# Optimization experiments

Hardware: AMD Instinct MI355X
Metric: run time of the kernel (lower is better)

Reference implementation:

```python
import math
import jax, jax.numpy as jnp
import numpy as np

D_MODEL = 1024
HEADS = 16
B, S = 4, 2048


def setup_inputs() -> dict:
    key = jax.random.key(0)
    ks = jax.random.split(key, 8)
    scale = 1.0 / math.sqrt(D_MODEL)
    return {
        "q": jax.random.normal(ks[0], (B, S, D_MODEL), dtype=jnp.float32),
        "k": jax.random.normal(ks[1], (B, S, D_MODEL), dtype=jnp.float32),
        "v": jax.random.normal(ks[2], (B, S, D_MODEL), dtype=jnp.float32),
        "mask": jax.random.randint(ks[3], (B, S), 0, 2).astype(jnp.bool_),
        "alibi_mask": jax.random.normal(ks[4], (1, HEADS, S, S), dtype=jnp.float32),
        "Wq": jax.random.normal(ks[5], (D_MODEL, D_MODEL), dtype=jnp.float32) * scale,
        "Wk": jax.random.normal(ks[6], (D_MODEL, D_MODEL), dtype=jnp.float32) * scale,
        "Wv": jax.random.normal(ks[7], (D_MODEL, D_MODEL), dtype=jnp.float32) * scale,
    }


def _split_heads(x):
    b, s, d = x.shape
    return x.reshape(b, s, HEADS, d // HEADS).transpose(0, 2, 1, 3)  # [B,H,S,hd]


def reference(q, k, v, mask, alibi_mask, Wq, Wk, Wv):
    # QKV projections (Linear, no bias)
    qh = _split_heads(q @ Wq)
    kh = _split_heads(k @ Wk)
    vh = _split_heads(v @ Wv)
    depth = qh.shape[-1]
    # naive full attention matrix [B,H,Sq,Sk]
    w = jnp.einsum("bhqd,bhkd->bhqk", qh, kh) / math.sqrt(depth)
    # mask: [B,Sk] -> [B,1,1,Sk], True = masked
    w = jnp.where(mask[:, None, None, :], -jnp.inf, w)
    w = w + alibi_mask
    a = jax.nn.softmax(w, axis=-1)  # dropout p=0 -> identity
    out = jnp.einsum("bhqk,bhkd->bhqd", a, vh)
    # combine heads -> [B,S,D]
    out = out.transpose(0, 2, 1, 3).reshape(q.shape[0], q.shape[1], -1)
    return (out, a)
```

## Files before the change

### kernel.cpp

```cpp
#include <hip/hip_runtime.h>
#include <hip/hip_bf16.h>
#include <math.h>

constexpr int B  = 4;
constexpr int S  = 2048;
constexpr int D  = 1024;
constexpr int H  = 16;
constexpr int HD = 64;
constexpr float SCALE = 0.125f;

using f32x4 = __attribute__((ext_vector_type(4))) float;
using s16x8 = __attribute__((ext_vector_type(8))) short;
using u16x8 = __attribute__((ext_vector_type(8))) unsigned short;
using u16x4 = __attribute__((ext_vector_type(4))) unsigned short;

__device__ __forceinline__ unsigned short f2bf(float f) {
    union { float f; unsigned u; } x; x.f = f;
    unsigned r = x.u + 0x7fffu + ((x.u >> 16) & 1u);
    return (unsigned short)(r >> 16);
}
__device__ __forceinline__ float bf2f(unsigned short h) {
    union { unsigned u; float f; } x; x.u = ((unsigned)h) << 16;
    return x.f;
}

#define MFMA_BF16(Af, Bf, Cf) __builtin_amdgcn_mfma_f32_16x16x32_bf16(Af, Bf, Cf, 0, 0, 0)

__global__ __launch_bounds__(256) void k_wt(const float* __restrict__ W,
                                            unsigned short* __restrict__ Wt) {
    __shared__ unsigned short T[64][68];
    const int k0 = blockIdx.x * 64, n0 = blockIdx.y * 64;
    const int t = threadIdx.x;
    {
        const int kr = t >> 4, nc4 = (t & 15) * 4;
        for (int rr = 0; rr < 4; ++rr) {
            const int kk = kr + rr * 16;
            f32x4 wv = *reinterpret_cast<const f32x4*>(&W[(size_t)(k0 + kk) * D + n0 + nc4]);
#pragma unroll
            for (int j = 0; j < 4; ++j) T[nc4 + j][kk] = f2bf(wv[j]);
        }
    }
    __syncthreads();
    {
        const int nr = t >> 4, kc4 = (t & 15) * 4;
        for (int rr = 0; rr < 4; ++rr) {
            const int nn = nr + rr * 16;
            u16x4 o;
#pragma unroll
            for (int j = 0; j < 4; ++j) o[j] = T[nn][kc4 + j];
            *reinterpret_cast<u16x4*>(&Wt[(size_t)(n0 + nn) * D + k0 + kc4]) = o;
        }
    }
}

__global__ __launch_bounds__(256) void k_proj_mfma(const float* __restrict__ X,
                                                   const unsigned short* __restrict__ Wt,
                                                   unsigned short* __restrict__ Y) {
    __shared__ alignas(16) unsigned short As[128][72];
    __shared__ alignas(16) unsigned short Bs[128][72];
    const int bm = blockIdx.y * 128, bn = blockIdx.x * 128;
    const int t = threadIdx.x, w = t >> 6, l = t & 63;
    const int wr = w >> 1, wc = w & 1;
    const int lr = l & 15, lg = l >> 4;
    f32x4 acc[4][4] = {};

    for (int k0 = 0; k0 < D; k0 += 64) {
        {
            const int c4 = (t & 15) * 4;
            int row = t >> 4;
            for (int rr = 0; rr < 8; ++rr, row += 16) {
                f32x4 xv = *reinterpret_cast<const f32x4*>(&X[(size_t)(bm + row) * D + k0 + c4]);
                u16x4 hv;
#pragma unroll
                for (int j = 0; j < 4; ++j) hv[j] = f2bf(xv[j]);
                *reinterpret_cast<u16x4*>(&As[row][c4]) = hv;
            }
        }
        for (int i = 0; i < 4; ++i) {
            const int idx = t + i * 256;
            const int row = idx >> 3, c8 = (idx & 7) * 8;
            *reinterpret_cast<u16x8*>(&Bs[row][c8]) =
                *reinterpret_cast<const u16x8*>(&Wt[(size_t)(bn + row) * D + k0 + c8]);
        }
        __syncthreads();
#pragma unroll
        for (int kk = 0; kk < 2; ++kk) {
            s16x8 af[4], bf[4];
#pragma unroll
            for (int f = 0; f < 4; ++f) {
                af[f] = *reinterpret_cast<const s16x8*>(&As[wr * 64 + f * 16 + lr][kk * 32 + lg * 8]);
                bf[f] = *reinterpret_cast<const s16x8*>(&Bs[wc * 64 + f * 16 + lr][kk * 32 + lg * 8]);
            }
#pragma unroll
            for (int fm = 0; fm < 4; ++fm)
#pragma unroll
                for (int fn = 0; fn < 4; ++fn)
                    acc[fm][fn] = MFMA_BF16(af[fm], bf[fn], acc[fm][fn]);
        }
        __syncthreads();
    }
#pragma unroll
    for (int fm = 0; fm < 4; ++fm)
#pragma unroll
        for (int fn = 0; fn < 4; ++fn)
#pragma unroll
            for (int r = 0; r < 4; ++r) {
                const int m = bm + wr * 64 + fm * 16 + lg * 4 + r;
                const int n = bn + wc * 64 + fn * 16 + lr;
                const int b = m >> 11, s = m & (S - 1);
                const int h = n >> 6, e = n & 63;
                Y[(((size_t)(b * H + h) * S) + s) * HD + e] = f2bf(acc[fm][fn][r]);
            }
}

__global__ __launch_bounds__(256) void k_vt(const unsigned short* __restrict__ Vh,
                                            unsigned short* __restrict__ VT) {
    __shared__ alignas(16) unsigned short T[64][264];
    const int bh = blockIdx.y;
    const int s0 = blockIdx.x * 256;
    const int t = threadIdx.x;
    {
        const int e4 = (t & 15) * 4;
        int sr = t >> 4;
        for (int rr = 0; rr < 16; ++rr, sr += 16) {
            u16x4 vv = *reinterpret_cast<const u16x4*>(&Vh[((size_t)bh * S + s0 + sr) * HD + e4]);
#pragma unroll
            for (int j = 0; j < 4; ++j) T[e4 + j][sr] = vv[j];
        }
    }
    __syncthreads();
    {
        const int e = t >> 2, sl0 = (t & 3) * 64;
        for (int c = 0; c < 8; ++c) {
            u16x8 o = *reinterpret_cast<const u16x8*>(&T[e][sl0 + c * 8]);
            *reinterpret_cast<u16x8*>(&VT[((size_t)bh * HD + e) * S + s0 + sl0 + c * 8]) = o;
        }
    }
}

__global__ __launch_bounds__(256) void k_abf16(const float* __restrict__ A,
                                               unsigned short* __restrict__ O) {
    const size_t N = (size_t)H * S * S;
    const size_t stride = (size_t)gridDim.x * 256 * 8;
    for (size_t i = ((size_t)blockIdx.x * 256 + threadIdx.x) * 8; i < N; i += stride) {
        f32x4 a0 = *reinterpret_cast<const f32x4*>(&A[i]);
        f32x4 a1 = *reinterpret_cast<const f32x4*>(&A[i + 4]);
        u16x8 o;
#pragma unroll
        for (int j = 0; j < 4; ++j) { o[j] = f2bf(a0[j]); o[4 + j] = f2bf(a1[j]); }
        *reinterpret_cast<u16x8*>(&O[i]) = o;
    }
}

template <bool ABF16>
__global__ __launch_bounds__(512, 4) void k_sumexp(
    const unsigned short* __restrict__ QH, const unsigned short* __restrict__ KH,
    const float* __restrict__ ALIBI, const unsigned short* __restrict__ ABF,
    const int* __restrict__ MASK, float* __restrict__ INVL) {
    __shared__ alignas(16) unsigned short Ks[64][72];
    __shared__ alignas(16) unsigned short ALs[128][72];

    const int bh = blockIdx.y, b = bh >> 4, h = bh & 15;
    const int q0 = blockIdx.x * 128;
    const int t = threadIdx.x, w = t >> 6, ln = t & 63;
    const int lr = ln & 15, lg = ln >> 4;

    const unsigned short* Qb = QH + (size_t)bh * S * HD;
    const unsigned short* Kb = KH + (size_t)bh * S * HD;
    const size_t hoff = (size_t)h * S * S;

    s16x8 qf[2];
#pragma unroll
    for (int kk = 0; kk < 2; ++kk)
        qf[kk] = *reinterpret_cast<const s16x8*>(
            &Qb[(size_t)(q0 + w * 16 + lr) * HD + kk * 32 + lg * 8]);

    float psum[4] = {0.f, 0.f, 0.f, 0.f};

    for (int k0 = 0; k0 < S; k0 += 64) {
        {
            const int row = t >> 3, c8 = (t & 7) * 8;
            *reinterpret_cast<u16x8*>(&Ks[row][c8]) =
                *reinterpret_cast<const u16x8*>(&Kb[(size_t)(k0 + row) * HD + c8]);
        }
#pragma unroll
        for (int i = 0; i < 2; ++i) {
            const int idx = t + i * 512, row = idx >> 3, c8 = (idx & 7) * 8;
            u16x8 av;
            if constexpr (ABF16) {
                av = *reinterpret_cast<const u16x8*>(&ABF[hoff + (size_t)(q0 + row) * S + k0 + c8]);
            } else {
                f32x4 a0 = *reinterpret_cast<const f32x4*>(&ALIBI[hoff + (size_t)(q0 + row) * S + k0 + c8]);
                f32x4 a1 = *reinterpret_cast<const f32x4*>(&ALIBI[hoff + (size_t)(q0 + row) * S + k0 + c8 + 4]);
#pragma unroll
                for (int j = 0; j < 4; ++j) { av[j] = f2bf(a0[j]); av[4 + j] = f2bf(a1[j]); }
            }
            *reinterpret_cast<u16x8*>(&ALs[row][c8]) = av;
        }
        float madd[4];
#pragma unroll
        for (int fn = 0; fn < 4; ++fn)
            madd[fn] = MASK[b * S + k0 + fn * 16 + lr] ? -1e30f : 0.f;
        __syncthreads();

        f32x4 acc[4] = {};
#pragma unroll
        for (int kk = 0; kk < 2; ++kk)
#pragma unroll
            for (int fn = 0; fn < 4; ++fn) {
                s16x8 kf = *reinterpret_cast<const s16x8*>(&Ks[fn * 16 + lr][kk * 32 + lg * 8]);
                acc[fn] = MFMA_BF16(qf[kk], kf, acc[fn]);
            }
#pragma unroll
        for (int r = 0; r < 4; ++r) {
            const int rowl = w * 16 + lg * 4 + r;
            float s = 0.f;
#pragma unroll
            for (int fn = 0; fn < 4; ++fn)
                s += __expf(fmaf(acc[fn][r], SCALE, bf2f(ALs[rowl][fn * 16 + lr]) + madd[fn]));
            psum[r] += s;
        }
        __syncthreads();
    }

#pragma unroll
    for (int r = 0; r < 4; ++r) {
        float ps = psum[r];
#pragma unroll
        for (int off = 1; off < 16; off <<= 1) ps += __shfl_xor(ps, off, 64);
        if (lr == 0)
            INVL[(size_t)bh * S + q0 + w * 16 + lg * 4 + r] = 1.0f / ps;
    }
}

template <bool ABF16>
__global__ __launch_bounds__(512, 2) void k_attn(
    const unsigned short* __restrict__ QH, const unsigned short* __restrict__ KH,
    const unsigned short* __restrict__ VT, const float* __restrict__ ALIBI,
    const unsigned short* __restrict__ ABF, const int* __restrict__ MASK,
    const float* __restrict__ INVL, float* __restrict__ Aout,
    float* __restrict__ OUT) {
    __shared__ alignas(16) unsigned short Ps[128][72];
    __shared__ alignas(16) unsigned short Ks[64][72];
    __shared__ alignas(16) unsigned short Vs[64][72];
    __shared__ alignas(16) unsigned short ALs[128][72];

    const int bh = blockIdx.y, b = bh >> 4, h = bh & 15;
    const int q0 = blockIdx.x * 128;
    const int t = threadIdx.x, w = t >> 6, ln = t & 63;
    const int lr = ln & 15, lg = ln >> 4;

    const unsigned short* Qb = QH + (size_t)bh * S * HD;
    const unsigned short* Kb = KH + (size_t)bh * S * HD;
    const unsigned short* Vb = VT + (size_t)bh * HD * S;
    const size_t hoff = (size_t)h * S * S;

    s16x8 qf[2];
#pragma unroll
    for (int kk = 0; kk < 2; ++kk)
        qf[kk] = *reinterpret_cast<const s16x8*>(
            &Qb[(size_t)(q0 + w * 16 + lr) * HD + kk * 32 + lg * 8]);

    float invl[4];
#pragma unroll
    for (int r = 0; r < 4; ++r)
        invl[r] = INVL[(size_t)bh * S + q0 + w * 16 + lg * 4 + r];

    f32x4 oacc[4] = {};
    for (int k0 = 0; k0 < S; k0 += 64) {
        {
            const int row = t >> 3, c8 = (t & 7) * 8;
            *reinterpret_cast<u16x8*>(&Ks[row][c8]) =
                *reinterpret_cast<const u16x8*>(&Kb[(size_t)(k0 + row) * HD + c8]);
            *reinterpret_cast<u16x8*>(&Vs[row][c8]) =
                *reinterpret_cast<const u16x8*>(&Vb[(size_t)row * S + k0 + c8]);
        }
#pragma unroll
        for (int i = 0; i < 2; ++i) {
            const int idx = t + i * 512, row = idx >> 3, c8 = (idx & 7) * 8;
            u16x8 av;
            if constexpr (ABF16) {
                av = *reinterpret_cast<const u16x8*>(&ABF[hoff + (size_t)(q0 + row) * S + k0 + c8]);
            } else {
                f32x4 a0 = *reinterpret_cast<const f32x4*>(&ALIBI[hoff + (size_t)(q0 + row) * S + k0 + c8]);
                f32x4 a1 = *reinterpret_cast<const f32x4*>(&ALIBI[hoff + (size_t)(q0 + row) * S + k0 + c8 + 4]);
#pragma unroll
                for (int j = 0; j < 4; ++j) { av[j] = f2bf(a0[j]); av[4 + j] = f2bf(a1[j]); }
            }
            *reinterpret_cast<u16x8*>(&ALs[row][c8]) = av;
        }
        float madd[4];
#pragma unroll
        for (int fn = 0; fn < 4; ++fn)
            madd[fn] = MASK[b * S + k0 + fn * 16 + lr] ? -1e30f : 0.f;
        __syncthreads();

        f32x4 acc[4] = {};
#pragma unroll
        for (int kk = 0; kk < 2; ++kk)
#pragma unroll
            for (int fn = 0; fn < 4; ++fn) {
                s16x8 kf = *reinterpret_cast<const s16x8*>(&Ks[fn * 16 + lr][kk * 32 + lg * 8]);
                acc[fn] = MFMA_BF16(qf[kk], kf, acc[fn]);
            }
#pragma unroll
        for (int r = 0; r < 4; ++r) {
            const int rowl = w * 16 + lg * 4 + r;
#pragma unroll
            for (int fn = 0; fn < 4; ++fn) {
                float p = __expf(fmaf(acc[fn][r], SCALE,
                                      bf2f(ALs[rowl][fn * 16 + lr]) + madd[fn])) * invl[r];
                Ps[rowl][fn * 16 + lr] = f2bf(p);
            }
        }
        __syncthreads();

#pragma unroll
        for (int i = 0; i < 2; ++i) {
            const int idx = t + i * 512, row = idx >> 3, sub = idx & 7;
            u16x8 pv = *reinterpret_cast<const u16x8*>(&Ps[row][sub * 8]);
            f32x4 o0, o1;
#pragma unroll
            for (int j = 0; j < 4; ++j) { o0[j] = bf2f(pv[j]); o1[j] = bf2f(pv[4 + j]); }
            float* dst = &Aout[((size_t)bh * S + q0 + row) * S + k0 + sub * 8];
            *reinterpret_cast<f32x4*>(dst) = o0;
            *reinterpret_cast<f32x4*>(dst + 4) = o1;
        }
#pragma unroll
        for (int c = 0; c < 2; ++c) {
            s16x8 pa = *reinterpret_cast<const s16x8*>(&Ps[w * 16 + lr][c * 32 + lg * 8]);
#pragma unroll
            for (int fn = 0; fn < 4; ++fn) {
                s16x8 vf = *reinterpret_cast<const s16x8*>(&Vs[fn * 16 + lr][c * 32 + lg * 8]);
                oacc[fn] = MFMA_BF16(pa, vf, oacc[fn]);
            }
        }
        __syncthreads();
    }

#pragma unroll
    for (int fn = 0; fn < 4; ++fn)
#pragma unroll
        for (int r = 0; r < 4; ++r)
            OUT[(size_t)(b * S + q0 + w * 16 + lg * 4 + r) * D + h * HD + fn * 16 + lr] =
                oacc[fn][r];
}

extern "C" void kernel_launch(void* const* d_in, const int* in_sizes, int n_in,
                              void* d_out, int out_size, void* d_ws, size_t ws_size,
                              hipStream_t stream) {
    const float* q     = (const float*)d_in[0];
    const float* k     = (const float*)d_in[1];
    const float* v     = (const float*)d_in[2];
    const int*   mask  = (const int*)d_in[3];
    const float* alibi = (const float*)d_in[4];
    const float* Wq    = (const float*)d_in[5];
    const float* Wk    = (const float*)d_in[6];
    const float* Wv    = (const float*)d_in[7];

    float* out = (float*)d_out;
    float* a   = out + (size_t)B * S * D;

    const size_t NH = (size_t)B * H * S * HD;
    unsigned short* qh  = (unsigned short*)d_ws;
    unsigned short* kh  = qh + NH;
    unsigned short* vh  = kh + NH;
    unsigned short* vT  = vh + NH;
    unsigned short* wqt = vT + NH;
    unsigned short* wkt = wqt + (size_t)D * D;
    unsigned short* wvt = wkt + (size_t)D * D;
    float*          invl = (float*)(wvt + (size_t)D * D);
    unsigned short* abf  = (unsigned short*)(invl + (size_t)B * H * S);

    const size_t need_bf16 =
        ((size_t)((unsigned short*)abf - qh) + (size_t)H * S * S) * sizeof(unsigned short);
    const bool use_abf16 = ws_size >= need_bf16;

    const dim3 blk(256);

    k_wt<<<dim3(D / 64, D / 64), blk, 0, stream>>>(Wq, wqt);
    k_wt<<<dim3(D / 64, D / 64), blk, 0, stream>>>(Wk, wkt);
    k_wt<<<dim3(D / 64, D / 64), blk, 0, stream>>>(Wv, wvt);

    if (use_abf16)
        k_abf16<<<dim3(8192), blk, 0, stream>>>(alibi, abf);

    k_proj_mfma<<<dim3(D / 128, (B * S) / 128), blk, 0, stream>>>(q, wqt, qh);
    k_proj_mfma<<<dim3(D / 128, (B * S) / 128), blk, 0, stream>>>(k, wkt, kh);
    k_proj_mfma<<<dim3(D / 128, (B * S) / 128), blk, 0, stream>>>(v, wvt, vh);

    k_vt<<<dim3(S / 256, B * H), blk, 0, stream>>>(vh, vT);

    if (use_abf16) {
        k_sumexp<true><<<dim3(S / 128, B * H), dim3(512), 0, stream>>>(
            qh, kh, alibi, abf, mask, invl);
        k_attn<true><<<dim3(S / 128, B * H), dim3(512), 0, stream>>>(
            qh, kh, vT, alibi, abf, mask, invl, a, out);
    } else {
        k_sumexp<false><<<dim3(S / 128, B * H), dim3(512), 0, stream>>>(
            qh, kh, alibi, abf, mask, invl);
        k_attn<false><<<dim3(S / 128, B * H), dim3(512), 0, stream>>>(
            qh, kh, vT, alibi, abf, mask, invl, a, out);
    }
}
```

Before: 714.3 us.

## Fuse V transpose into projection, batch-share alibi in sumexp, double-buffer attention

The V projection now writes its transposed layout directly through shared memory, which removes the separate transpose kernel and the intermediate V buffer. The sumexp kernel walks all four batches for each head and query tile, so each alibi tile is read and converted once and shared across batches. That kernel also writes the bf16 alibi copy itself, replacing the standalone conversion kernel. The attention kernel double-buffers K/V tiles, remaps block indices into an XCD-aware order, raises the occupancy hint, and writes the probability matrix with nontemporal fp32 stores straight from registers. In exchange, sumexp launches only 256 blocks, which may leave compute units underused, and it holds more registers for four query fragment sets.

```diff
diff --git a/kernel.cpp b/kernel.cpp
--- a/kernel.cpp
+++ b/kernel.cpp
@@ -113,225 +113,279 @@
             }
 }
 
-__global__ __launch_bounds__(256) void k_vt(const unsigned short* __restrict__ Vh,
-                                            unsigned short* __restrict__ VT) {
-    __shared__ alignas(16) unsigned short T[64][264];
-    const int bh = blockIdx.y;
-    const int s0 = blockIdx.x * 256;
-    const int t = threadIdx.x;
-    {
-        const int e4 = (t & 15) * 4;
-        int sr = t >> 4;
-        for (int rr = 0; rr < 16; ++rr, sr += 16) {
-            u16x4 vv = *reinterpret_cast<const u16x4*>(&Vh[((size_t)bh * S + s0 + sr) * HD + e4]);
-#pragma unroll
-            for (int j = 0; j < 4; ++j) T[e4 + j][sr] = vv[j];
-        }
-    }
+__global__ __launch_bounds__(256) void k_projv_mfma(const float* __restrict__ X,
+                                                    const unsigned short* __restrict__ Wt,
+                                                    unsigned short* __restrict__ VT) {
+    __shared__ alignas(16) unsigned short SM[2][128][72];
+    unsigned short (*As)[72] = SM[0];
+    unsigned short (*Bs)[72] = SM[1];
+    const int bm = blockIdx.y * 128, bn = blockIdx.x * 128;
+    const int t = threadIdx.x, w = t >> 6, l = t & 63;
+    const int wr = w >> 1, wc = w & 1;
+    const int lr = l & 15, lg = l >> 4;
+    f32x4 acc[4][4] = {};
+
+    for (int k0 = 0; k0 < D; k0 += 64) {
+        {
+            const int c4 = (t & 15) * 4;
+            int row = t >> 4;
+            for (int rr = 0; rr < 8; ++rr, row += 16) {
+                f32x4 xv = *reinterpret_cast<const f32x4*>(&X[(size_t)(bm + row) * D + k0 + c4]);
+                u16x4 hv;
+#pragma unroll
+                for (int j = 0; j < 4; ++j) hv[j] = f2bf(xv[j]);
+                *reinterpret_cast<u16x4*>(&As[row][c4]) = hv;
+            }
+        }
+        for (int i = 0; i < 4; ++i) {
+            const int idx = t + i * 256;
+            const int row = idx >> 3, c8 = (idx & 7) * 8;
+            *reinterpret_cast<u16x8*>(&Bs[row][c8]) =
+                *reinterpret_cast<const u16x8*>(&Wt[(size_t)(bn + row) * D + k0 + c8]);
+        }
+        __syncthreads();
+#pragma unroll
+        for (int kk = 0; kk < 2; ++kk) {
+            s16x8 af[4], bf[4];
+#pragma unroll
+            for (int f = 0; f < 4; ++f) {
+                af[f] = *reinterpret_cast<const s16x8*>(&As[wr * 64 + f * 16 + lr][kk * 32 + lg * 8]);
+                bf[f] = *reinterpret_cast<const s16x8*>(&Bs[wc * 64 + f * 16 + lr][kk * 32 + lg * 8]);
+            }
+#pragma unroll
+            for (int fm = 0; fm < 4; ++fm)
+#pragma unroll
+                for (int fn = 0; fn < 4; ++fn)
+                    acc[fm][fn] = MFMA_BF16(af[fm], bf[fn], acc[fm][fn]);
+        }
+        __syncthreads();
+    }
+    unsigned short (*T)[144] = reinterpret_cast<unsigned short(*)[144]>(&SM[0][0][0]);
+#pragma unroll
+    for (int fm = 0; fm < 4; ++fm)
+#pragma unroll
+        for (int fn = 0; fn < 4; ++fn)
+#pragma unroll
+            for (int r = 0; r < 4; ++r)
+                T[wc * 64 + fn * 16 + lr][wr * 64 + fm * 16 + lg * 4 + r] = f2bf(acc[fm][fn][r]);
     __syncthreads();
-    {
-        const int e = t >> 2, sl0 = (t & 3) * 64;
-        for (int c = 0; c < 8; ++c) {
-            u16x8 o = *reinterpret_cast<const u16x8*>(&T[e][sl0 + c * 8]);
-            *reinterpret_cast<u16x8*>(&VT[((size_t)bh * HD + e) * S + s0 + sl0 + c * 8]) = o;
-        }
-    }
-}
-
-__global__ __launch_bounds__(256) void k_abf16(const float* __restrict__ A,
-                                               unsigned short* __restrict__ O) {
-    const size_t N = (size_t)H * S * S;
-    const size_t stride = (size_t)gridDim.x * 256 * 8;
-    for (size_t i = ((size_t)blockIdx.x * 256 + threadIdx.x) * 8; i < N; i += stride) {
-        f32x4 a0 = *reinterpret_cast<const f32x4*>(&A[i]);
-        f32x4 a1 = *reinterpret_cast<const f32x4*>(&A[i + 4]);
-        u16x8 o;
-#pragma unroll
-        for (int j = 0; j < 4; ++j) { o[j] = f2bf(a0[j]); o[4 + j] = f2bf(a1[j]); }
-        *reinterpret_cast<u16x8*>(&O[i]) = o;
+    const int b = bm >> 11, s0 = bm & (S - 1);
+    for (int it = 0; it < 8; ++it) {
+        const int idx = t + it * 256;
+        const int row = idx >> 4, c8 = (idx & 15) * 8;
+        const int h = (bn + row) >> 6, e = (bn + row) & 63;
+        *reinterpret_cast<u16x8*>(&VT[((size_t)(b * H + h) * HD + e) * S + s0 + c8]) =
+            *reinterpret_cast<const u16x8*>(&T[row][c8]);
     }
 }
 
 template <bool ABF16>
 __global__ __launch_bounds__(512, 4) void k_sumexp(
     const unsigned short* __restrict__ QH, const unsigned short* __restrict__ KH,
-    const float* __restrict__ ALIBI, const unsigned short* __restrict__ ABF,
+    const float* __restrict__ ALIBI, unsigned short* __restrict__ ABF,
     const int* __restrict__ MASK, float* __restrict__ INVL) {
-    __shared__ alignas(16) unsigned short Ks[64][72];
-    __shared__ alignas(16) unsigned short ALs[128][72];
-
-    const int bh = blockIdx.y, b = bh >> 4, h = bh & 15;
-    const int q0 = blockIdx.x * 128;
+    __shared__ alignas(16) unsigned short Ks[2][64][72];
+    __shared__ alignas(16) unsigned short ALs[2][128][72];
+
+    const int bid = blockIdx.x;
+    const int wg = (bid & 7) * 32 + (bid >> 3);
+    const int h = wg >> 4;
+    const int q0 = (wg & 15) * 128;
     const int t = threadIdx.x, w = t >> 6, ln = t & 63;
     const int lr = ln & 15, lg = ln >> 4;
-
-    const unsigned short* Qb = QH + (size_t)bh * S * HD;
-    const unsigned short* Kb = KH + (size_t)bh * S * HD;
     const size_t hoff = (size_t)h * S * S;
 
-    s16x8 qf[2];
-#pragma unroll
-    for (int kk = 0; kk < 2; ++kk)
-        qf[kk] = *reinterpret_cast<const s16x8*>(
-            &Qb[(size_t)(q0 + w * 16 + lr) * HD + kk * 32 + lg * 8]);
-
-    float psum[4] = {0.f, 0.f, 0.f, 0.f};
-
-    for (int k0 = 0; k0 < S; k0 += 64) {
-        {
-            const int row = t >> 3, c8 = (t & 7) * 8;
-            *reinterpret_cast<u16x8*>(&Ks[row][c8]) =
-                *reinterpret_cast<const u16x8*>(&Kb[(size_t)(k0 + row) * HD + c8]);
-        }
+    s16x8 qf[4][2];
+#pragma unroll
+    for (int b = 0; b < 4; ++b)
+#pragma unroll
+        for (int kk = 0; kk < 2; ++kk)
+            qf[b][kk] = *reinterpret_cast<const s16x8*>(
+                &QH[((size_t)(b * H + h) * S + q0 + w * 16 + lr) * HD + kk * 32 + lg * 8]);
+
+    auto stage_k = [&](int buf, int b, int k0) {
+        const int row = t >> 3, c8 = (t & 7) * 8;
+        *reinterpret_cast<u16x8*>(&Ks[buf][row][c8]) =
+            *reinterpret_cast<const u16x8*>(
+                &KH[((size_t)(b * H + h) * S + k0 + row) * HD + c8]);
+    };
+    auto stage_al = [&](int buf, int k0) {
 #pragma unroll
         for (int i = 0; i < 2; ++i) {
             const int idx = t + i * 512, row = idx >> 3, c8 = (idx & 7) * 8;
+            const size_t goff = hoff + (size_t)(q0 + row) * S + k0 + c8;
+            f32x4 a0 = *reinterpret_cast<const f32x4*>(&ALIBI[goff]);
+            f32x4 a1 = *reinterpret_cast<const f32x4*>(&ALIBI[goff + 4]);
             u16x8 av;
-            if constexpr (ABF16) {
-                av = *reinterpret_cast<const u16x8*>(&ABF[hoff + (size_t)(q0 + row) * S + k0 + c8]);
-            } else {
-                f32x4 a0 = *reinterpret_cast<const f32x4*>(&ALIBI[hoff + (size_t)(q0 + row) * S + k0 + c8]);
-                f32x4 a1 = *reinterpret_cast<const f32x4*>(&ALIBI[hoff + (size_t)(q0 + row) * S + k0 + c8 + 4]);
-#pragma unroll
-                for (int j = 0; j < 4; ++j) { av[j] = f2bf(a0[j]); av[4 + j] = f2bf(a1[j]); }
-            }
-            *reinterpret_cast<u16x8*>(&ALs[row][c8]) = av;
-        }
-        float madd[4];
-#pragma unroll
-        for (int fn = 0; fn < 4; ++fn)
-            madd[fn] = MASK[b * S + k0 + fn * 16 + lr] ? -1e30f : 0.f;
-        __syncthreads();
-
-        f32x4 acc[4] = {};
-#pragma unroll
-        for (int kk = 0; kk < 2; ++kk)
-#pragma unroll
-            for (int fn = 0; fn < 4; ++fn) {
-                s16x8 kf = *reinterpret_cast<const s16x8*>(&Ks[fn * 16 + lr][kk * 32 + lg * 8]);
-                acc[fn] = MFMA_BF16(qf[kk], kf, acc[fn]);
-            }
+#pragma unroll
+            for (int j = 0; j < 4; ++j) { av[j] = f2bf(a0[j]); av[4 + j] = f2bf(a1[j]); }
+            *reinterpret_cast<u16x8*>(&ALs[buf][row][c8]) = av;
+            if constexpr (ABF16)
+                *reinterpret_cast<u16x8*>(&ABF[goff]) = av;
+        }
+    };
+
+    float psum[4][4] = {};
+
+    stage_k(0, 0, 0);
+    stage_al(0, 0);
+    __syncthreads();
+
+    for (int t16 = 0; t16 < 32; ++t16) {
+        const int k0 = t16 * 64;
+        const int acur = t16 & 1;
+#pragma unroll
+        for (int b = 0; b < 4; ++b) {
+            const int kcur = b & 1;
+            if (b < 3) stage_k(kcur ^ 1, b + 1, k0);
+            else if (t16 < 31) stage_k(kcur ^ 1, 0, k0 + 64);
+            if (b == 0 && t16 < 31) stage_al(acur ^ 1, k0 + 64);
+
+            float madd[4];
+#pragma unroll
+            for (int fn = 0; fn < 4; ++fn)
+                madd[fn] = MASK[b * S + k0 + fn * 16 + lr] ? -1e30f : 0.f;
+
+            f32x4 acc[4] = {};
+#pragma unroll
+            for (int kk = 0; kk < 2; ++kk)
+#pragma unroll
+                for (int fn = 0; fn < 4; ++fn) {
+                    s16x8 kf = *reinterpret_cast<const s16x8*>(&Ks[kcur][fn * 16 + lr][kk * 32 + lg * 8]);
+                    acc[fn] = MFMA_BF16(qf[b][kk], kf, acc[fn]);
+                }
+#pragma unroll
+            for (int r = 0; r < 4; ++r) {
+                const int rowl = w * 16 + lg * 4 + r;
+                float s = 0.f;
+#pragma unroll
+                for (int fn = 0; fn < 4; ++fn)
+                    s += __expf(fmaf(acc[fn][r], SCALE,
+                                     bf2f(ALs[acur][rowl][fn * 16 + lr]) + madd[fn]));
+                psum[b][r] += s;
+            }
+            __syncthreads();
+        }
+    }
+
+#pragma unroll
+    for (int b = 0; b < 4; ++b)
 #pragma unroll
         for (int r = 0; r < 4; ++r) {
-            const int rowl = w * 16 + lg * 4 + r;
-            float s = 0.f;
-#pragma unroll
-            for (int fn = 0; fn < 4; ++fn)
-                s += __expf(fmaf(acc[fn][r], SCALE, bf2f(ALs[rowl][fn * 16 + lr]) + madd[fn]));
-            psum[r] += s;
-        }
-        __syncthreads();
-    }
-
-#pragma unroll
-    for (int r = 0; r < 4; ++r) {
-        float ps = psum[r];
-#pragma unroll
-        for (int off = 1; off < 16; off <<= 1) ps += __shfl_xor(ps, off, 64);
-        if (lr == 0)
-            INVL[(size_t)bh * S + q0 + w * 16 + lg * 4 + r] = 1.0f / ps;
-    }
+            float ps = psum[b][r];
+#pragma unroll
+            for (int off = 1; off < 16; off <<= 1) ps += __shfl_xor(ps, off, 64);
+            if (lr == 0)
+                INVL[(size_t)(b * H + h) * S + q0 + w * 16 + lg * 4 + r] = 1.0f / ps;
+        }
 }
 
 template <bool ABF16>
-__global__ __launch_bounds__(512, 2) void k_attn(
+__global__ __launch_bounds__(512, 4) void k_attn(
     const unsigned short* __restrict__ QH, const unsigned short* __restrict__ KH,
     const unsigned short* __restrict__ VT, const float* __restrict__ ALIBI,
     const unsigned short* __restrict__ ABF, const int* __restrict__ MASK,
     const float* __restrict__ INVL, float* __restrict__ Aout,
     float* __restrict__ OUT) {
+    __shared__ alignas(16) unsigned short Ks[2][64][72];
+    __shared__ alignas(16) unsigned short Vs[2][64][72];
+    __shared__ alignas(16) unsigned short ALs[128][72];
     __shared__ alignas(16) unsigned short Ps[128][72];
-    __shared__ alignas(16) unsigned short Ks[64][72];
-    __shared__ alignas(16) unsigned short Vs[64][72];
-    __shared__ alignas(16) unsigned short ALs[128][72];
-
-    const int bh = blockIdx.y, b = bh >> 4, h = bh & 15;
-    const int q0 = blockIdx.x * 128;
+
+    const int bid = blockIdx.x;
+    const int wg = (bid & 7) * 128 + (bid >> 3);
+    const int bh = wg >> 4, b = bh >> 4, h = bh & 15;
+    const int q0 = (wg & 15) * 128;
     const int t = threadIdx.x, w = t >> 6, ln = t & 63;
     const int lr = ln & 15, lg = ln >> 4;
-
-    const unsigned short* Qb = QH + (size_t)bh * S * HD;
+    const size_t hoff = (size_t)h * S * S;
+
     const unsigned short* Kb = KH + (size_t)bh * S * HD;
     const unsigned short* Vb = VT + (size_t)bh * HD * S;
-    const size_t hoff = (size_t)h * S * S;
 
     s16x8 qf[2];
 #pragma unroll
     for (int kk = 0; kk < 2; ++kk)
         qf[kk] = *reinterpret_cast<const s16x8*>(
-            &Qb[(size_t)(q0 + w * 16 + lr) * HD + kk * 32 + lg * 8]);
+            &QH[((size_t)bh * S + q0 + w * 16 + lr) * HD + kk * 32 + lg * 8]);
 
     float invl[4];
 #pragma unroll
     for (int r = 0; r < 4; ++r)
         invl[r] = INVL[(size_t)bh * S + q0 + w * 16 + lg * 4 + r];
 
-    f32x4 oacc[4] = {};
-    for (int k0 = 0; k0 < S; k0 += 64) {
-        {
-            const int row = t >> 3, c8 = (t & 7) * 8;
-            *reinterpret_cast<u16x8*>(&Ks[row][c8]) =
-                *reinterpret_cast<const u16x8*>(&Kb[(size_t)(k0 + row) * HD + c8]);
-            *reinterpret_cast<u16x8*>(&Vs[row][c8]) =
-                *reinterpret_cast<const u16x8*>(&Vb[(size_t)row * S + k0 + c8]);
-        }
+    auto stage_kv = [&](int buf, int k0) {
+        const int row = t >> 3, c8 = (t & 7) * 8;
+        *reinterpret_cast<u16x8*>(&Ks[buf][row][c8]) =
+            *reinterpret_cast<const u16x8*>(&Kb[(size_t)(k0 + row) * HD + c8]);
+        *reinterpret_cast<u16x8*>(&Vs[buf][row][c8]) =
+            *reinterpret_cast<const u16x8*>(&Vb[(size_t)row * S + k0 + c8]);
+    };
+    auto stage_al = [&](int k0) {
 #pragma unroll
         for (int i = 0; i < 2; ++i) {
-            const int idx = t + i * 512, row = idx >> 3, c8 = (idx & 7) * 8;
+            const int rowl = w * 16 + (ln >> 3) + i * 8;
+            const int c8 = (ln & 7) * 8;
             u16x8 av;
             if constexpr (ABF16) {
-                av = *reinterpret_cast<const u16x8*>(&ABF[hoff + (size_t)(q0 + row) * S + k0 + c8]);
+                av = *reinterpret_cast<const u16x8*>(
+                    &ABF[hoff + (size_t)(q0 + rowl) * S + k0 + c8]);
             } else {
-                f32x4 a0 = *reinterpret_cast<const f32x4*>(&ALIBI[hoff + (size_t)(q0 + row) * S + k0 + c8]);
-                f32x4 a1 = *reinterpret_cast<const f32x4*>(&ALIBI[hoff + (size_t)(q0 + row) * S + k0 + c8 + 4]);
+                const size_t goff = hoff + (size_t)(q0 + rowl) * S + k0 + c8;
+                f32x4 a0 = *reinterpret_cast<const f32x4*>(&ALIBI[goff]);
+                f32x4 a1 = *reinterpret_cast<const f32x4*>(&ALIBI[goff + 4]);
 #pragma unroll
                 for (int j = 0; j < 4; ++j) { av[j] = f2bf(a0[j]); av[4 + j] = f2bf(a1[j]); }
             }
-            *reinterpret_cast<u16x8*>(&ALs[row][c8]) = av;
-        }
+            *reinterpret_cast<u16x8*>(&ALs[rowl][c8]) = av;
+        }
+    };
+
+    f32x4 oacc[4] = {};
+
+    stage_kv(0, 0);
+    stage_al(0);
+    __syncthreads();
+
+    for (int t16 = 0; t16 < 32; ++t16) {
+        const int k0 = t16 * 64, cur = t16 & 1;
+        if (t16 < 31) stage_kv(cur ^ 1, k0 + 64);
+
         float madd[4];
 #pragma unroll
         for (int fn = 0; fn < 4; ++fn)
             madd[fn] = MASK[b * S + k0 + fn * 16 + lr] ? -1e30f : 0.f;
-        __syncthreads();
 
         f32x4 acc[4] = {};
 #pragma unroll
         for (int kk = 0; kk < 2; ++kk)
 #pragma unroll
             for (int fn = 0; fn < 4; ++fn) {
-                s16x8 kf = *reinterpret_cast<const s16x8*>(&Ks[fn * 16 + lr][kk * 32 + lg * 8]);
+                s16x8 kf = *reinterpret_cast<const s16x8*>(&Ks[cur][fn * 16 + lr][kk * 32 + lg * 8]);
                 acc[fn] = MFMA_BF16(qf[kk], kf, acc[fn]);
             }
+
 #pragma unroll
         for (int r = 0; r < 4; ++r) {
             const int rowl = w * 16 + lg * 4 + r;
+            float* arow = Aout + ((size_t)bh * S + q0 + rowl) * S + k0;
 #pragma unroll
             for (int fn = 0; fn < 4; ++fn) {
                 float p = __expf(fmaf(acc[fn][r], SCALE,
                                       bf2f(ALs[rowl][fn * 16 + lr]) + madd[fn])) * invl[r];
                 Ps[rowl][fn * 16 + lr] = f2bf(p);
-            }
-        }
-        __syncthreads();
-
-#pragma unroll
-        for (int i = 0; i < 2; ++i) {
-            const int idx = t + i * 512, row = idx >> 3, sub = idx & 7;
-            u16x8 pv = *reinterpret_cast<const u16x8*>(&Ps[row][sub * 8]);
-            f32x4 o0, o1;
-#pragma unroll
-            for (int j = 0; j < 4; ++j) { o0[j] = bf2f(pv[j]); o1[j] = bf2f(pv[4 + j]); }
-            float* dst = &Aout[((size_t)bh * S + q0 + row) * S + k0 + sub * 8];
-            *reinterpret_cast<f32x4*>(dst) = o0;
-            *reinterpret_cast<f32x4*>(dst + 4) = o1;
-        }
+                __builtin_nontemporal_store(p, arow + fn * 16 + lr);
+            }
+        }
+
+        if (t16 < 31) stage_al(k0 + 64);
+
 #pragma unroll
         for (int c = 0; c < 2; ++c) {
             s16x8 pa = *reinterpret_cast<const s16x8*>(&Ps[w * 16 + lr][c * 32 + lg * 8]);
 #pragma unroll
             for (int fn = 0; fn < 4; ++fn) {
-                s16x8 vf = *reinterpret_cast<const s16x8*>(&Vs[fn * 16 + lr][c * 32 + lg * 8]);
+                s16x8 vf = *reinterpret_cast<const s16x8*>(&Vs[cur][fn * 16 + lr][c * 32 + lg * 8]);
                 oacc[fn] = MFMA_BF16(pa, vf, oacc[fn]);
             }
         }
@@ -364,8 +418,7 @@
     const size_t NH = (size_t)B * H * S * HD;
     unsigned short* qh  = (unsigned short*)d_ws;
     unsigned short* kh  = qh + NH;
-    unsigned short* vh  = kh + NH;
-    unsigned short* vT  = vh + NH;
+    unsigned short* vT  = kh + NH;
     unsigned short* wqt = vT + NH;
     unsigned short* wkt = wqt + (size_t)D * D;
     unsigned short* wvt = wkt + (size_t)D * D;
@@ -373,7 +426,7 @@
     unsigned short* abf  = (unsigned short*)(invl + (size_t)B * H * S);
 
     const size_t need_bf16 =
-        ((size_t)((unsigned short*)abf - qh) + (size_t)H * S * S) * sizeof(unsigned short);
+        ((size_t)(abf - qh) + (size_t)H * S * S) * sizeof(unsigned short);
     const bool use_abf16 = ws_size >= need_bf16;
 
     const dim3 blk(256);
@@ -382,24 +435,17 @@
     k_wt<<<dim3(D / 64, D / 64), blk, 0, stream>>>(Wk, wkt);
     k_wt<<<dim3(D / 64, D / 64), blk, 0, stream>>>(Wv, wvt);
 
-    if (use_abf16)
-        k_abf16<<<dim3(8192), blk, 0, stream>>>(alibi, abf);
-
     k_proj_mfma<<<dim3(D / 128, (B * S) / 128), blk, 0, stream>>>(q, wqt, qh);
     k_proj_mfma<<<dim3(D / 128, (B * S) / 128), blk, 0, stream>>>(k, wkt, kh);
-    k_proj_mfma<<<dim3(D / 128, (B * S) / 128), blk, 0, stream>>>(v, wvt, vh);
-
-    k_vt<<<dim3(S / 256, B * H), blk, 0, stream>>>(vh, vT);
+    k_projv_mfma<<<dim3(D / 128, (B * S) / 128), blk, 0, stream>>>(v, wvt, vT);
 
     if (use_abf16) {
-        k_sumexp<true><<<dim3(S / 128, B * H), dim3(512), 0, stream>>>(
-            qh, kh, alibi, abf, mask, invl);
-        k_attn<true><<<dim3(S / 128, B * H), dim3(512), 0, stream>>>(
+        k_sumexp<true><<<dim3(256), dim3(512), 0, stream>>>(qh, kh, alibi, abf, mask, invl);
+        k_attn<true><<<dim3(1024), dim3(512), 0, stream>>>(
             qh, kh, vT, alibi, abf, mask, invl, a, out);
     } else {
-        k_sumexp<false><<<dim3(S / 128, B * H), dim3(512), 0, stream>>>(
-            qh, kh, alibi, abf, mask, invl);
-        k_attn<false><<<dim3(S / 128, B * H), dim3(512), 0, stream>>>(
+        k_sumexp<false><<<dim3(256), dim3(512), 0, stream>>>(qh, kh, alibi, abf, mask, invl);
+        k_attn<false><<<dim3(1024), dim3(512), 0, stream>>>(
             qh, kh, vT, alibi, abf, mask, invl, a, out);
     }
 }
```

Result: slower. 961.2 us (+34.6%).
